# Kernel optimization log

Hardware: AMD Instinct MI355X
Metric: run time of the kernel (lower is better)

## Reference

```python
import jax, jax.numpy as jnp
import numpy as np

SIZE = (4096, 4096)   # self.size
SIGMA = 1.0           # blur_sigma
NOISE_STD = 0.01      # noise_std


def _gauss_kernel(sigma):
    # scipy.ndimage.gaussian_filter: radius = int(truncate*sigma + 0.5), truncate=4.0
    r = int(4.0 * sigma + 0.5)
    x = np.arange(-r, r + 1, dtype=np.float32)
    k = np.exp(-0.5 * (x / sigma) ** 2)
    k = k / k.sum()
    return jnp.asarray(k), r


def _blur(img, sigma):
    # img: [C, H, W]; separable Gaussian, scipy mode='reflect' == jnp symmetric pad
    k, r = _gauss_kernel(sigma)
    x = jnp.pad(img, ((0, 0), (r, r), (r, r)), mode='symmetric')
    x = x[:, None]  # [C, 1, H+2r, W+2r] (NCHW)
    kh = k.reshape(1, 1, -1, 1)
    kw = k.reshape(1, 1, 1, -1)
    x = jax.lax.conv_general_dilated(x, kh, (1, 1), 'VALID')
    x = jax.lax.conv_general_dilated(x, kw, (1, 1), 'VALID')
    return x[:, 0]  # [C, H, W]


def setup_inputs() -> dict:
    key = jax.random.key(0)
    k1, k2 = jax.random.split(key)
    img = jax.random.normal(k1, (1, 2048, 2048), dtype=jnp.float32)
    noise = jax.random.normal(k2, (1,) + SIZE, dtype=jnp.float32)
    return {"img": img, "noise": noise}


def reference(img, noise):
    # bilinear resize, align_corners=False == jax half-pixel linear resize
    img = jax.image.resize(img, (img.shape[0],) + SIZE, method='linear')
    img = jnp.flip(img, axis=2)   # horizontal flip
    img = jnp.flip(img, axis=1)   # vertical flip
    img = jnp.rot90(img, k=1, axes=(1, 2))  # rot90, k fixed to 1
    img = img + noise * NOISE_STD
    img = _blur(img, SIGMA)
    img = jnp.log1p(jnp.clip(img, 0.0))  # clamp(min=0) then log1p
    return img
```

## Files before the change

kernel.cpp:

```cpp
#include <hip/hip_runtime.h>
#include <math.h>

#define N      4096
#define NIMG   2048
#define TXO    56
#define HR     40
#define DRS    48
#define IPP    27
#define IPR    34
#define NSX    74
#define NSY    103
#define NSTRIP (NSX * NSY)
#define NBLK   ((NSTRIP + 3) / 4)

#define KW0 0.00013383063f
#define KW1 0.00443186160f
#define KW2 0.05399112800f
#define KW3 0.24197144000f
#define KW4 0.39894346870f

__device__ __forceinline__ int symi(int g) {
    g = (g < 0) ? (-1 - g) : g;
    g = (g >= N) ? (2 * N - 1 - g) : g;
    return g;
}


#define PRODUCE8(M, OFS, NZA, NOFS)                                            \
    do {                                                                       \
        if (yin) {                                                             \
            const int ab_ = a0 + 4 * (M);                                      \
            float g0 = fmaf(wr0, IP[ab_ + 0], wr1 * IP[ab_ + IPP + 0]);        \
            float g1 = fmaf(wr0, IP[ab_ + 1], wr1 * IP[ab_ + IPP + 1]);        \
            float g2 = fmaf(wr0, IP[ab_ + 2], wr1 * IP[ab_ + IPP + 2]);        \
            float g3 = fmaf(wr0, IP[ab_ + 3], wr1 * IP[ab_ + IPP + 3]);        \
            float g4 = fmaf(wr0, IP[ab_ + 4], wr1 * IP[ab_ + IPP + 4]);        \
            float g5 = fmaf(wr0, IP[ab_ + 5], wr1 * IP[ab_ + IPP + 5]);        \
            win[(OFS) + 0] = fmaf(0.25f, g0, fmaf(0.75f, g1, 0.01f * (NZA)[(NOFS) + 0])); \
            win[(OFS) + 1] = fmaf(0.75f, g1, fmaf(0.25f, g2, 0.01f * (NZA)[(NOFS) + 1])); \
            win[(OFS) + 2] = fmaf(0.25f, g1, fmaf(0.75f, g2, 0.01f * (NZA)[(NOFS) + 2])); \
            win[(OFS) + 3] = fmaf(0.75f, g2, fmaf(0.25f, g3, 0.01f * (NZA)[(NOFS) + 3])); \
            win[(OFS) + 4] = fmaf(0.25f, g2, fmaf(0.75f, g3, 0.01f * (NZA)[(NOFS) + 4])); \
            win[(OFS) + 5] = fmaf(0.75f, g3, fmaf(0.25f, g4, 0.01f * (NZA)[(NOFS) + 5])); \
            win[(OFS) + 6] = fmaf(0.25f, g3, fmaf(0.75f, g4, 0.01f * (NZA)[(NOFS) + 6])); \
            win[(OFS) + 7] = fmaf(0.75f, g4, fmaf(0.25f, g5, 0.01f * (NZA)[(NOFS) + 7])); \
        } else {                                                               \
            _Pragma("unroll")                                                  \
            for (int j_ = 0; j_ < 8; ++j_) {                                   \
                const int dr_  = 8 * (M) + j_;                                 \
                const int gym_ = symi(y0 - 4 + dr_);                           \
                const int jc_  = ((gym_ - 1) >> 1) - c0min;                    \
                const float wc1_ = (gym_ & 1) ? 0.25f : 0.75f;                 \
                const float wc0_ = 1.0f - wc1_;                                \
                const float f0_ = IP[a0 + jc_],       f1_ = IP[a0 + jc_ + 1];  \
                const float f2_ = IP[a0 + IPP + jc_], f3_ = IP[a0 + IPP + jc_ + 1]; \
                const float top_ = fmaf(wc0_, f0_, wc1_ * f1_);                \
                const float bot_ = fmaf(wc0_, f2_, wc1_ * f3_);                \
                win[(OFS) + j_] = fmaf(0.01f, (NZA)[(NOFS) + j_],              \
                                       fmaf(wr0, top_, wr1 * bot_));           \
            }                                                                  \
        }                                                                      \
    } while (0)

__global__ __launch_bounds__(256, 6)
void TensorAugment_79216376807666_kernel(const float* __restrict__ img,
                                         const float* __restrict__ noise,
                                         float* __restrict__ out) {
    __shared__ float SH[4 * IPR * IPP];

    const int tid  = threadIdx.x;
    const int lane = tid & 63;
    const int wave = tid >> 6;

    float* const IP = SH + wave * (IPR * IPP);

    const int strip0 = blockIdx.x * 4 + wave;
    if (strip0 >= NSTRIP) return;

    const int strip = __builtin_amdgcn_readfirstlane(strip0);
    const int sx = strip % NSX;
    const int sy = strip / NSX;
    const int x0 = sx * TXO;
    const int y0 = sy * HR;
    const bool yin = (sy > 0) && (sy < NSY - 1);

    int gxa = x0 - 4, gxb = x0 + 59;
    int mxa = symi(gxa), mxb = symi(gxb);
    int gxmin = min(mxa, mxb), gxmax = max(mxa, mxb);
    if (gxa <= 0) gxmin = 0;
    if (gxb >= N - 1) gxmax = N - 1;
    int umin = (N - 1) - gxmax, umax = (N - 1) - gxmin;
    int r0min = (umin - 1) >> 1;
    int r0max = (umax - 1) >> 1;
    int nrows = r0max - r0min + 2;

    int gya = y0 - 4, gyb = y0 + DRS - 5;
    int mya = symi(gya), myb = symi(gyb);
    int gymin = min(mya, myb), gymax = max(mya, myb);
    if (gya <= 0) gymin = 0;
    if (gyb >= N - 1) gymax = N - 1;
    int c0min = (gymin - 1) >> 1;
    int c0max = (gymax - 1) >> 1;
    int ncols = c0max - c0min + 2;

    {
        const int c  = lane & 31;
        const int rb = lane >> 5;
        const bool cok = (c < ncols);
#pragma unroll
        for (int k = 0; k < 17; ++k) {
            const int r = rb + 2 * k;
            if (cok && r < nrows) {
                const int ir = min(max(r0min + r, 0), NIMG - 1);
                const int ic = min(max(c0min + c, 0), NIMG - 1);
                IP[r * IPP + c] = img[ir * NIMG + ic];
            }
        }
    }

    const int gx  = x0 - 4 + lane;
    const int gxm = symi(gx);
    const int u   = (N - 1) - gxm;
    const int r0  = (u - 1) >> 1;
    const float wr1 = (u & 1) ? 0.25f : 0.75f;
    const float wr0 = 1.0f - wr1;
    const int a0  = (r0 - r0min) * IPP;
    const bool oklane = (lane >= 4) && (lane < 60) && (gx < N);

    int ba[9];
#pragma unroll
    for (int d = 0; d < 9; ++d) ba[d] = 4 * (lane + d - 4);

    const float* const nzb = noise + ((size_t)max(y0 - 4, 0) * N + gxm);

    float win[16];
    {
        float nzp[16];
        if (yin) {
#pragma unroll
            for (int j = 0; j < 16; ++j) nzp[j] = nzb[(size_t)j * N];
        } else {
#pragma unroll
            for (int j = 0; j < 16; ++j)
                nzp[j] = noise[(size_t)symi(y0 - 4 + j) * N + gxm];
        }
        PRODUCE8(0, 0, nzp, 0);
        PRODUCE8(1, 8, nzp, 8);
    }

#pragma unroll 1
    for (int ck = 2; ck <= 6; ++ck) {
        float nz8[8];
        if (ck < 6) {
            if (yin) {
                const float* nr = nzb + (size_t)(8 * ck) * N;
#pragma unroll
                for (int j = 0; j < 8; ++j) nz8[j] = nr[(size_t)j * N];
            } else {
#pragma unroll
                for (int j = 0; j < 8; ++j)
                    nz8[j] = noise[(size_t)symi(y0 - 4 + 8 * ck + j) * N + gxm];
            }
        }

        const int gyb0 = y0 + 8 * (ck - 2);
#pragma unroll
        for (int j = 0; j < 8; ++j) {
            float v = KW0 * win[j];
            v = fmaf(KW1, win[j + 1], v);
            v = fmaf(KW2, win[j + 2], v);
            v = fmaf(KW3, win[j + 3], v);
            v = fmaf(KW4, win[j + 4], v);
            v = fmaf(KW3, win[j + 5], v);
            v = fmaf(KW2, win[j + 6], v);
            v = fmaf(KW1, win[j + 7], v);
            v = fmaf(KW0, win[j + 8], v);
            const int vi = __float_as_int(v);
            float acc = KW4 * v;
            acc = fmaf(KW0, __int_as_float(__builtin_amdgcn_ds_bpermute(ba[0], vi)), acc);
            acc = fmaf(KW1, __int_as_float(__builtin_amdgcn_ds_bpermute(ba[1], vi)), acc);
            acc = fmaf(KW2, __int_as_float(__builtin_amdgcn_ds_bpermute(ba[2], vi)), acc);
            acc = fmaf(KW3, __int_as_float(__builtin_amdgcn_ds_bpermute(ba[3], vi)), acc);
            acc = fmaf(KW3, __int_as_float(__builtin_amdgcn_ds_bpermute(ba[5], vi)), acc);
            acc = fmaf(KW2, __int_as_float(__builtin_amdgcn_ds_bpermute(ba[6], vi)), acc);
            acc = fmaf(KW1, __int_as_float(__builtin_amdgcn_ds_bpermute(ba[7], vi)), acc);
            acc = fmaf(KW0, __int_as_float(__builtin_amdgcn_ds_bpermute(ba[8], vi)), acc);
            acc = fmaxf(acc, 0.0f);
            const float r = __logf(1.0f + acc);
            const int gy = gyb0 + j;
            if (oklane && gy < N) out[(size_t)gy * N + gx] = r;
        }

        if (ck < 6) {
#pragma unroll
            for (int i = 0; i < 8; ++i) win[i] = win[i + 8];
            PRODUCE8(ck, 8, nz8, 0);
        }
    }
}

extern "C" void kernel_launch(void* const* d_in, const int* in_sizes, int n_in,
                              void* d_out, int out_size, void* d_ws, size_t ws_size,
                              hipStream_t stream) {
    const float* img   = (const float*)d_in[0];
    const float* noise = (const float*)d_in[1];
    float* out = (float*)d_out;

    dim3 grid(NBLK);
    TensorAugment_79216376807666_kernel<<<grid, 256, 0, stream>>>(img, noise, out);
}
```

Measured before the change: 145.9 us.

## Shrink per-wave strip height to 24 rows and fully unroll column loop

Reduces each wave's vertical strip from 40 to 24 output rows, which adjusts the shared-memory image patch pitch and raises the strip count. The chunk loop is fully unrolled into three explicit output stages, and launch bounds go up to 8 waves per SIMD for higher occupancy. The aim is more parallelism and fewer loop overheads. The cost is a larger share of vertical halo work, since 8 extra rows are computed per 24 instead of per 40, which means more redundant noise reads and interpolation.

```diff
diff --git a/kernel.cpp b/kernel.cpp
--- a/kernel.cpp
+++ b/kernel.cpp
@@ -4,12 +4,12 @@
 #define N      4096
 #define NIMG   2048
 #define TXO    56
-#define HR     40
-#define DRS    48
-#define IPP    27
+#define HR     24
+#define DRS    32
+#define IPP    19
 #define IPR    34
 #define NSX    74
-#define NSY    103
+#define NSY    171
 #define NSTRIP (NSX * NSY)
 #define NBLK   ((NSTRIP + 3) / 4)
 
@@ -62,7 +62,43 @@
         }                                                                      \
     } while (0)
 
-__global__ __launch_bounds__(256, 6)
+#define OUT8(GY0)                                                              \
+    do {                                                                       \
+        _Pragma("unroll")                                                      \
+        for (int j = 0; j < 8; ++j) {                                          \
+            float v = KW0 * win[j];                                            \
+            v = fmaf(KW1, win[j + 1], v);                                      \
+            v = fmaf(KW2, win[j + 2], v);                                      \
+            v = fmaf(KW3, win[j + 3], v);                                      \
+            v = fmaf(KW4, win[j + 4], v);                                      \
+            v = fmaf(KW3, win[j + 5], v);                                      \
+            v = fmaf(KW2, win[j + 6], v);                                      \
+            v = fmaf(KW1, win[j + 7], v);                                      \
+            v = fmaf(KW0, win[j + 8], v);                                      \
+            const int vi = __float_as_int(v);                                  \
+            float acc = KW4 * v;                                               \
+            acc = fmaf(KW0, __int_as_float(__builtin_amdgcn_ds_bpermute(ba[0], vi)), acc); \
+            acc = fmaf(KW1, __int_as_float(__builtin_amdgcn_ds_bpermute(ba[1], vi)), acc); \
+            acc = fmaf(KW2, __int_as_float(__builtin_amdgcn_ds_bpermute(ba[2], vi)), acc); \
+            acc = fmaf(KW3, __int_as_float(__builtin_amdgcn_ds_bpermute(ba[3], vi)), acc); \
+            acc = fmaf(KW3, __int_as_float(__builtin_amdgcn_ds_bpermute(ba[5], vi)), acc); \
+            acc = fmaf(KW2, __int_as_float(__builtin_amdgcn_ds_bpermute(ba[6], vi)), acc); \
+            acc = fmaf(KW1, __int_as_float(__builtin_amdgcn_ds_bpermute(ba[7], vi)), acc); \
+            acc = fmaf(KW0, __int_as_float(__builtin_amdgcn_ds_bpermute(ba[8], vi)), acc); \
+            acc = fmaxf(acc, 0.0f);                                            \
+            const float r = __logf(1.0f + acc);                                \
+            const int gy = (GY0) + j;                                          \
+            if (oklane && gy < N) out[(size_t)gy * N + gx] = r;                \
+        }                                                                      \
+    } while (0)
+
+#define SLIDE8()                                                               \
+    do {                                                                       \
+        _Pragma("unroll")                                                      \
+        for (int i_ = 0; i_ < 8; ++i_) win[i_] = win[i_ + 8];                  \
+    } while (0)
+
+__global__ __launch_bounds__(256, 8)
 void TensorAugment_79216376807666_kernel(const float* __restrict__ img,
                                          const float* __restrict__ noise,
                                          float* __restrict__ out) {
@@ -148,55 +184,39 @@
         PRODUCE8(1, 8, nzp, 8);
     }
 
-#pragma unroll 1
-    for (int ck = 2; ck <= 6; ++ck) {
-        float nz8[8];
-        if (ck < 6) {
-            if (yin) {
-                const float* nr = nzb + (size_t)(8 * ck) * N;
-#pragma unroll
-                for (int j = 0; j < 8; ++j) nz8[j] = nr[(size_t)j * N];
-            } else {
-#pragma unroll
-                for (int j = 0; j < 8; ++j)
-                    nz8[j] = noise[(size_t)symi(y0 - 4 + 8 * ck + j) * N + gxm];
-            }
-        }
-
-        const int gyb0 = y0 + 8 * (ck - 2);
-#pragma unroll
-        for (int j = 0; j < 8; ++j) {
-            float v = KW0 * win[j];
-            v = fmaf(KW1, win[j + 1], v);
-            v = fmaf(KW2, win[j + 2], v);
-            v = fmaf(KW3, win[j + 3], v);
-            v = fmaf(KW4, win[j + 4], v);
-            v = fmaf(KW3, win[j + 5], v);
-            v = fmaf(KW2, win[j + 6], v);
-            v = fmaf(KW1, win[j + 7], v);
-            v = fmaf(KW0, win[j + 8], v);
-            const int vi = __float_as_int(v);
-            float acc = KW4 * v;
-            acc = fmaf(KW0, __int_as_float(__builtin_amdgcn_ds_bpermute(ba[0], vi)), acc);
-            acc = fmaf(KW1, __int_as_float(__builtin_amdgcn_ds_bpermute(ba[1], vi)), acc);
-            acc = fmaf(KW2, __int_as_float(__builtin_amdgcn_ds_bpermute(ba[2], vi)), acc);
-            acc = fmaf(KW3, __int_as_float(__builtin_amdgcn_ds_bpermute(ba[3], vi)), acc);
-            acc = fmaf(KW3, __int_as_float(__builtin_amdgcn_ds_bpermute(ba[5], vi)), acc);
-            acc = fmaf(KW2, __int_as_float(__builtin_amdgcn_ds_bpermute(ba[6], vi)), acc);
-            acc = fmaf(KW1, __int_as_float(__builtin_amdgcn_ds_bpermute(ba[7], vi)), acc);
-            acc = fmaf(KW0, __int_as_float(__builtin_amdgcn_ds_bpermute(ba[8], vi)), acc);
-            acc = fmaxf(acc, 0.0f);
-            const float r = __logf(1.0f + acc);
-            const int gy = gyb0 + j;
-            if (oklane && gy < N) out[(size_t)gy * N + gx] = r;
-        }
-
-        if (ck < 6) {
-#pragma unroll
-            for (int i = 0; i < 8; ++i) win[i] = win[i + 8];
-            PRODUCE8(ck, 8, nz8, 0);
-        }
-    }
+    {
+        float nzA[8];
+        if (yin) {
+            const float* nr = nzb + (size_t)16 * N;
+#pragma unroll
+            for (int j = 0; j < 8; ++j) nzA[j] = nr[(size_t)j * N];
+        } else {
+#pragma unroll
+            for (int j = 0; j < 8; ++j)
+                nzA[j] = noise[(size_t)symi(y0 + 12 + j) * N + gxm];
+        }
+        OUT8(y0);
+        SLIDE8();
+        PRODUCE8(2, 8, nzA, 0);
+    }
+
+    {
+        float nzB[8];
+        if (yin) {
+            const float* nr = nzb + (size_t)24 * N;
+#pragma unroll
+            for (int j = 0; j < 8; ++j) nzB[j] = nr[(size_t)j * N];
+        } else {
+#pragma unroll
+            for (int j = 0; j < 8; ++j)
+                nzB[j] = noise[(size_t)symi(y0 + 20 + j) * N + gxm];
+        }
+        OUT8(y0 + 8);
+        SLIDE8();
+        PRODUCE8(3, 8, nzB, 0);
+    }
+
+    OUT8(y0 + 16);
 }
 
 extern "C" void kernel_launch(void* const* d_in, const int* in_sizes, int n_in,
```

Result: no change. 148.4 us (+1.8%).
